# Optimization experiments

Hardware: AMD Instinct MI355X
Metric: run time of the kernel (lower is better)

## Reference

```python
import jax, jax.numpy as jnp
import numpy as np

ITERS = 3          # num_iterations
EPS_ATTN = 1e-8    # epsilon offset on attention
LN_EPS = 1e-5      # torch LayerNorm default eps


def _ln(x, g, b):
    m = x.mean(-1, keepdims=True)
    v = ((x - m) ** 2).mean(-1, keepdims=True)
    return (x - m) * jax.lax.rsqrt(v + LN_EPS) * g + b


def setup_inputs() -> dict:
    key = jax.random.key(0)
    ks = jax.random.split(key, 16)
    B, N, D, S, H = 64, 4096, 64, 8, 128

    def lin_w(k, fan_in, fan_out):
        lim = (1.0 / fan_in) ** 0.5
        return jax.random.uniform(k, (fan_in, fan_out), minval=-lim, maxval=lim, dtype=jnp.float32)

    def lin_b(k, fan_in, fan_out):
        lim = (1.0 / fan_in) ** 0.5
        return jax.random.uniform(k, (fan_out,), minval=-lim, maxval=lim, dtype=jnp.float32)

    return {
        "inputs": jax.random.normal(ks[0], (B, N, D), dtype=jnp.float32),
        "noise": jax.random.normal(ks[1], (B, S, D), dtype=jnp.float32),
        "slots_mu": jax.random.normal(ks[2], (1, 1, D), dtype=jnp.float32),
        "slots_log_sigma": jax.random.uniform(ks[3], (1, 1, D), minval=-0.3, maxval=0.3, dtype=jnp.float32),
        "wq": lin_w(ks[4], D, D), "bq": lin_b(ks[4], D, D),
        "wk": lin_w(ks[5], D, D), "bk": lin_b(ks[5], D, D),
        "wv": lin_w(ks[6], D, D), "bv": lin_b(ks[6], D, D),
        "w_ih": lin_w(ks[7], D, 3 * D), "b_ih": lin_b(ks[7], D, 3 * D),
        "w_hh": lin_w(ks[8], D, 3 * D), "b_hh": lin_b(ks[8], D, 3 * D),
        "w1": lin_w(ks[9], D, H), "b1": lin_b(ks[9], D, H),
        "w2": lin_w(ks[10], H, D), "b2": lin_b(ks[10], H, D),
        "g_in": jnp.ones((D,), jnp.float32), "beta_in": jnp.zeros((D,), jnp.float32),
        "g_sl": jnp.ones((D,), jnp.float32), "beta_sl": jnp.zeros((D,), jnp.float32),
        "g_ff": jnp.ones((D,), jnp.float32), "beta_ff": jnp.zeros((D,), jnp.float32),
    }


def reference(inputs, noise, slots_mu, slots_log_sigma, wq, bq, wk, bk, wv, bv,
              w_ih, b_ih, w_hh, b_hh, w1, b1, w2, b2,
              g_in, beta_in, g_sl, beta_sl, g_ff, beta_ff):
    b, n, d = inputs.shape
    scale = d ** -0.5

    slots = slots_mu + jnp.exp(slots_log_sigma) * noise          # [b, S, d]
    x = _ln(inputs, g_in, beta_in)
    k = x @ wk + bk                                              # [b, n, d]
    v = x @ wv + bv                                              # [b, n, d]

    for _ in range(ITERS):
        slots_prev = slots
        q = _ln(slots, g_sl, beta_sl) @ wq + bq                  # [b, S, d]
        dots = jnp.einsum('bid,bjd->bij', q, k) * scale          # [b, S, n]
        attn = jax.nn.softmax(dots, axis=1) + EPS_ATTN           # softmax over slots
        attn = attn / attn.sum(-1, keepdims=True)                # renorm over inputs
        updates = jnp.einsum('bjd,bij->bid', v, attn)            # [b, S, d]

        # GRUCell (torch gate order: reset, update, new)
        gx = updates @ w_ih + b_ih
        gh = slots_prev @ w_hh + b_hh
        xr, xz, xn = jnp.split(gx, 3, axis=-1)
        hr, hz, hn = jnp.split(gh, 3, axis=-1)
        r = jax.nn.sigmoid(xr + hr)
        z = jax.nn.sigmoid(xz + hz)
        nw = jnp.tanh(xn + r * hn)
        slots = (1.0 - z) * nw + z * slots_prev

        # residual MLP
        ff = _ln(slots, g_ff, beta_ff)
        slots = slots + (jax.nn.relu(ff @ w1 + b1) @ w2 + b2)
    return slots
```

## Files before the change

### kernel.cpp

```cpp
#include <hip/hip_runtime.h>
#include <math.h>

#define LN_EPS 1e-5f
#define EPS_ATTN 1e-8f
#define SCALE 0.125f
#define CHUNKS 32

__device__ __forceinline__ float wsum64(float v) {
#pragma unroll
  for (int m = 1; m <= 32; m <<= 1) v += __shfl_xor(v, m, 64);
  return v;
}

__device__ __forceinline__ float red16(float v) {
  v += __int_as_float(__builtin_amdgcn_update_dpp(0, __float_as_int(v), 0xB1, 0xF, 0xF, true));
  v += __int_as_float(__builtin_amdgcn_update_dpp(0, __float_as_int(v), 0x4E, 0xF, 0xF, true));
  v += __int_as_float(__builtin_amdgcn_update_dpp(0, __float_as_int(v), 0x124, 0xF, 0xF, true));
  v += __int_as_float(__builtin_amdgcn_update_dpp(0, __float_as_int(v), 0x128, 0xF, 0xF, true));
  return v;
}

__global__ __launch_bounds__(64) void k_init(
    const float* __restrict__ noise, const float* __restrict__ mu,
    const float* __restrict__ lsig,
    const float* __restrict__ wq, const float* __restrict__ bq,
    const float* __restrict__ wk, const float* __restrict__ bk,
    const float* __restrict__ g_sl, const float* __restrict__ beta_sl,
    float* __restrict__ S_buf, float* __restrict__ qk, float* __restrict__ qb,
    float* __restrict__ acc, float* __restrict__ asum,
    float* __restrict__ M, float* __restrict__ cvec,
    float* __restrict__ uvec, float* __restrict__ s0v)
{
  int bi = blockIdx.x;
  int lane = threadIdx.x;
  if (bi < 512) {
    float sl = mu[lane] + __expf(lsig[lane]) * noise[bi * 64 + lane];
    S_buf[bi * 64 + lane] = sl;
    acc[bi * 64 + lane] = 0.0f;
    if (lane == 0) asum[bi] = 0.0f;

    float s  = wsum64(sl);
    float s2 = wsum64(sl * sl);
    float mean = s * (1.0f / 64.0f);
    float var  = s2 * (1.0f / 64.0f) - mean * mean;
    float rstd = rsqrtf(var + LN_EPS);
    float ln = (sl - mean) * rstd * g_sl[lane] + beta_sl[lane];

    float q = bq[lane];
#pragma unroll
    for (int t = 0; t < 64; ++t) q += __shfl(ln, t, 64) * wq[t * 64 + lane];
    float qkl = 0.0f;
#pragma unroll
    for (int d = 0; d < 64; ++d) qkl += __shfl(q, d, 64) * wk[lane * 64 + d];
    qk[bi * 64 + lane] = qkl * SCALE;
    float qbl = wsum64(q * bk[lane]);
    if (lane == 0) qb[bi] = qbl * SCALE;
  } else if (bi < 576) {
    int t = bi - 512;
    float wqv = wq[t * 64 + lane];
    float m = 0.0f;
#pragma unroll
    for (int d = 0; d < 64; ++d) m += __shfl(wqv, d, 64) * wk[lane * 64 + d];
    M[t * 64 + lane] = m * SCALE;
    float uv = wsum64(wqv * bk[lane]);
    if (lane == 0) uvec[t] = uv * SCALE;
  } else {
    float bqv = bq[lane];
    float cc = 0.0f;
#pragma unroll
    for (int j = 0; j < 64; ++j) cc += __shfl(bqv, j, 64) * wk[lane * 64 + j];
    cvec[lane] = cc * SCALE;
    float ss = wsum64(bq[lane] * bk[lane]);
    if (lane == 0) s0v[0] = ss * SCALE;
  }
}

__global__ __launch_bounds__(256) void k_main(
    const float* __restrict__ inputs,
    const float* __restrict__ g_in, const float* __restrict__ beta_in,
    const float* __restrict__ qk, const float* __restrict__ qb,
    float* __restrict__ acc, float* __restrict__ asum)
{
  __shared__ float lds_qk[512];
  __shared__ float lds_qb[8];
  __shared__ float lds_acc[4][512];
  __shared__ float lds_as[4][8];
  const int b = blockIdx.y;
  const int chunk = blockIdx.x;
  const int tid = threadIdx.x;
  const int lane = tid & 63;
  const int wave = tid >> 6;
  const int p = lane & 15;

  if (tid < 128)
    ((float4*)lds_qk)[tid] = ((const float4*)(qk + b * 512))[tid];
  if (tid >= 128 && tid < 136)
    lds_qb[tid - 128] = qb[b * 8 + (tid - 128)];

  float4 g4  = ((const float4*)g_in)[p];
  float4 be4 = ((const float4*)beta_in)[p];

  float4 accl[8];
  float asl[8];
#pragma unroll
  for (int i = 0; i < 8; ++i) { accl[i] = make_float4(0.f, 0.f, 0.f, 0.f); asl[i] = 0.f; }

  __syncthreads();

  const float4* in4 = (const float4*)(inputs + (size_t)b * 4096 * 64);
  const float4* qk4 = (const float4*)lds_qk;
  const int rb0 = chunk * 128 + wave * 8;

  for (int it = 0; it < 4; ++it) {
    float4 xa = in4[(rb0 + it * 32) * 16 + lane];
    float4 xb = in4[(rb0 + it * 32 + 4) * 16 + lane];

    float sA  = red16(xa.x + xa.y + xa.z + xa.w);
    float s2A = red16(xa.x * xa.x + xa.y * xa.y + xa.z * xa.z + xa.w * xa.w);
    float meanA = sA * 0.015625f;
    float varA  = s2A * 0.015625f - meanA * meanA;
    float rstdA = rsqrtf(varA + LN_EPS);
    float4 xlnA;
    xlnA.x = (xa.x - meanA) * rstdA * g4.x + be4.x;
    xlnA.y = (xa.y - meanA) * rstdA * g4.y + be4.y;
    xlnA.z = (xa.z - meanA) * rstdA * g4.z + be4.z;
    xlnA.w = (xa.w - meanA) * rstdA * g4.w + be4.w;

    float sB  = red16(xb.x + xb.y + xb.z + xb.w);
    float s2B = red16(xb.x * xb.x + xb.y * xb.y + xb.z * xb.z + xb.w * xb.w);
    float meanB = sB * 0.015625f;
    float varB  = s2B * 0.015625f - meanB * meanB;
    float rstdB = rsqrtf(varB + LN_EPS);
    float4 xlnB;
    xlnB.x = (xb.x - meanB) * rstdB * g4.x + be4.x;
    xlnB.y = (xb.y - meanB) * rstdB * g4.y + be4.y;
    xlnB.z = (xb.z - meanB) * rstdB * g4.z + be4.z;
    xlnB.w = (xb.w - meanB) * rstdB * g4.w + be4.w;

    float pvA[8], pvB[8];
    float psA = 0.0f, psB = 0.0f;
#pragma unroll
    for (int i = 0; i < 8; ++i) {
      float4 qv = qk4[i * 16 + p];
      float qbi = lds_qb[i];
      float da = xlnA.x * qv.x + xlnA.y * qv.y + xlnA.z * qv.z + xlnA.w * qv.w;
      float db = xlnB.x * qv.x + xlnB.y * qv.y + xlnB.z * qv.z + xlnB.w * qv.w;
      da = red16(da) + qbi;
      db = red16(db) + qbi;
      float ea = __expf(da);
      float eb = __expf(db);
      pvA[i] = ea; psA += ea;
      pvB[i] = eb; psB += eb;
    }
    float invA = __builtin_amdgcn_rcpf(psA);
    float invB = __builtin_amdgcn_rcpf(psB);
#pragma unroll
    for (int i = 0; i < 8; ++i) {
      float ppa = pvA[i] * invA + EPS_ATTN;
      float ppb = pvB[i] * invB + EPS_ATTN;
      asl[i] += ppa + ppb;
      accl[i].x += ppa * xlnA.x; accl[i].x += ppb * xlnB.x;
      accl[i].y += ppa * xlnA.y; accl[i].y += ppb * xlnB.y;
      accl[i].z += ppa * xlnA.z; accl[i].z += ppb * xlnB.z;
      accl[i].w += ppa * xlnA.w; accl[i].w += ppb * xlnB.w;
    }
  }

#pragma unroll
  for (int i = 0; i < 8; ++i) {
#pragma unroll
    for (int m = 16; m <= 32; m <<= 1) {
      accl[i].x += __shfl_xor(accl[i].x, m, 64);
      accl[i].y += __shfl_xor(accl[i].y, m, 64);
      accl[i].z += __shfl_xor(accl[i].z, m, 64);
      accl[i].w += __shfl_xor(accl[i].w, m, 64);
      asl[i]    += __shfl_xor(asl[i], m, 64);
    }
  }

  if (lane < 16) {
    float4* dst = (float4*)lds_acc[wave];
#pragma unroll
    for (int i = 0; i < 8; ++i) dst[i * 16 + p] = accl[i];
  }
  if (lane == 0) {
#pragma unroll
    for (int i = 0; i < 8; ++i) lds_as[wave][i] = asl[i];
  }
  __syncthreads();

  for (int f = tid; f < 512; f += 256) {
    float ssum = lds_acc[0][f] + lds_acc[1][f] + lds_acc[2][f] + lds_acc[3][f];
    atomicAdd(&acc[b * 512 + f], ssum);
  }
  if (tid < 8) {
    float ssum = lds_as[0][tid] + lds_as[1][tid] + lds_as[2][tid] + lds_as[3][tid];
    atomicAdd(&asum[b * 8 + tid], ssum);
  }
}

__global__ __launch_bounds__(256) void k_update(
    const float* __restrict__ S_in, float* __restrict__ S_out,
    float* __restrict__ acc, float* __restrict__ asum,
    const float* __restrict__ wv, const float* __restrict__ bv,
    const float* __restrict__ w_ih, const float* __restrict__ b_ih,
    const float* __restrict__ w_hh, const float* __restrict__ b_hh,
    const float* __restrict__ w1, const float* __restrict__ b1,
    const float* __restrict__ w2, const float* __restrict__ b2,
    const float* __restrict__ g_ff, const float* __restrict__ beta_ff,
    const float* __restrict__ M, const float* __restrict__ cvec,
    const float* __restrict__ uvec, const float* __restrict__ s0v,
    const float* __restrict__ g_sl, const float* __restrict__ beta_sl,
    float* __restrict__ qk, float* __restrict__ qb, int do_next)
{
  __shared__ float red[6][4][64];
  const int bi   = blockIdx.x;
  const int tid  = threadIdx.x;
  const int lane = tid & 63;
  const int w    = tid >> 6;
  const int e0   = w * 16;

  float asv = asum[bi];
  float v   = acc[bi * 64 + lane] / asv;
  float sp  = S_in[bi * 64 + lane];

  float up = 0.0f;
#pragma unroll
  for (int e = 0; e < 16; ++e) {
    float vv = __shfl(v, e0 + e, 64);
    up += vv * wv[(e0 + e) * 64 + lane];
  }
  red[0][w][lane] = up;
  __syncthreads();
  float upd = bv[lane] + red[0][0][lane] + red[0][1][lane]
                       + red[0][2][lane] + red[0][3][lane];

  float gxr = 0, gxz = 0, gxn = 0, ghr = 0, ghz = 0, ghn = 0;
#pragma unroll
  for (int e = 0; e < 16; ++e) {
    int ee = e0 + e;
    float uu = __shfl(upd, ee, 64);
    float hh = __shfl(sp, ee, 64);
    const float* wi = w_ih + ee * 192;
    const float* wh = w_hh + ee * 192;
    gxr += uu * wi[lane]; gxz += uu * wi[64 + lane]; gxn += uu * wi[128 + lane];
    ghr += hh * wh[lane]; ghz += hh * wh[64 + lane]; ghn += hh * wh[128 + lane];
  }
  __syncthreads();
  red[0][w][lane] = gxr; red[1][w][lane] = gxz; red[2][w][lane] = gxn;
  red[3][w][lane] = ghr; red[4][w][lane] = ghz; red[5][w][lane] = ghn;
  __syncthreads();
  gxr = b_ih[lane]       + red[0][0][lane] + red[0][1][lane] + red[0][2][lane] + red[0][3][lane];
  gxz = b_ih[64 + lane]  + red[1][0][lane] + red[1][1][lane] + red[1][2][lane] + red[1][3][lane];
  gxn = b_ih[128 + lane] + red[2][0][lane] + red[2][1][lane] + red[2][2][lane] + red[2][3][lane];
  ghr = b_hh[lane]       + red[3][0][lane] + red[3][1][lane] + red[3][2][lane] + red[3][3][lane];
  ghz = b_hh[64 + lane]  + red[4][0][lane] + red[4][1][lane] + red[4][2][lane] + red[4][3][lane];
  ghn = b_hh[128 + lane] + red[5][0][lane] + red[5][1][lane] + red[5][2][lane] + red[5][3][lane];

  float r  = 1.0f / (1.0f + __expf(-(gxr + ghr)));
  float z  = 1.0f / (1.0f + __expf(-(gxz + ghz)));
  float nw = tanhf(gxn + r * ghn);
  float sn = (1.0f - z) * nw + z * sp;

  float s  = wsum64(sn);
  float s2 = wsum64(sn * sn);
  float mean = s * (1.0f / 64.0f);
  float var  = s2 * (1.0f / 64.0f) - mean * mean;
  float rstd = rsqrtf(var + LN_EPS);
  float ff = (sn - mean) * rstd * g_ff[lane] + beta_ff[lane];

  float h1 = 0.0f, h2 = 0.0f;
#pragma unroll
  for (int e = 0; e < 16; ++e) {
    int ee = e0 + e;
    float f = __shfl(ff, ee, 64);
    h1 += f * w1[ee * 128 + lane];
    h2 += f * w1[ee * 128 + 64 + lane];
  }
  __syncthreads();
  red[0][w][lane] = h1; red[1][w][lane] = h2;
  __syncthreads();
  h1 = fmaxf(b1[lane]      + red[0][0][lane] + red[0][1][lane] + red[0][2][lane] + red[0][3][lane], 0.0f);
  h2 = fmaxf(b1[64 + lane] + red[1][0][lane] + red[1][1][lane] + red[1][2][lane] + red[1][3][lane], 0.0f);

  float po = 0.0f;
#pragma unroll
  for (int t = 0; t < 16; ++t) {
    int tt = e0 + t;
    po += __shfl(h1, tt, 64) * w2[tt * 64 + lane];
    po += __shfl(h2, tt, 64) * w2[(64 + tt) * 64 + lane];
  }
  __syncthreads();
  red[0][w][lane] = po;
  __syncthreads();
  float o = sn + b2[lane] + red[0][0][lane] + red[0][1][lane]
                          + red[0][2][lane] + red[0][3][lane];
  if (w == 0) S_out[bi * 64 + lane] = o;

  if (do_next && w == 0) {
    acc[bi * 64 + lane] = 0.0f;
    if (lane == 0) asum[bi] = 0.0f;
  }

  if (do_next) {
    float so  = wsum64(o);
    float so2 = wsum64(o * o);
    float mo  = so * (1.0f / 64.0f);
    float vo  = so2 * (1.0f / 64.0f) - mo * mo;
    float ro  = rsqrtf(vo + LN_EPS);
    float ln  = (o - mo) * ro * g_sl[lane] + beta_sl[lane];

    float pq = 0.0f;
#pragma unroll
    for (int t = 0; t < 16; ++t) {
      int tt = e0 + t;
      pq += __shfl(ln, tt, 64) * M[tt * 64 + lane];
    }
    __syncthreads();
    red[1][w][lane] = pq;
    __syncthreads();
    if (w == 0) {
      qk[bi * 64 + lane] = cvec[lane] + red[1][0][lane] + red[1][1][lane]
                                      + red[1][2][lane] + red[1][3][lane];
      float pb = wsum64(ln * uvec[lane]);
      if (lane == 0) qb[bi] = s0v[0] + pb;
    }
  }
}

extern "C" void kernel_launch(void* const* d_in, const int* in_sizes, int n_in,
                              void* d_out, int out_size, void* d_ws, size_t ws_size,
                              hipStream_t stream) {
  const float* inputs  = (const float*)d_in[0];
  const float* noise   = (const float*)d_in[1];
  const float* mu      = (const float*)d_in[2];
  const float* lsig    = (const float*)d_in[3];
  const float* wq      = (const float*)d_in[4];
  const float* bq      = (const float*)d_in[5];
  const float* wk      = (const float*)d_in[6];
  const float* bk      = (const float*)d_in[7];
  const float* wv      = (const float*)d_in[8];
  const float* bv      = (const float*)d_in[9];
  const float* w_ih    = (const float*)d_in[10];
  const float* b_ih    = (const float*)d_in[11];
  const float* w_hh    = (const float*)d_in[12];
  const float* b_hh    = (const float*)d_in[13];
  const float* w1      = (const float*)d_in[14];
  const float* b1      = (const float*)d_in[15];
  const float* w2      = (const float*)d_in[16];
  const float* b2      = (const float*)d_in[17];
  const float* g_in    = (const float*)d_in[18];
  const float* beta_in = (const float*)d_in[19];
  const float* g_sl    = (const float*)d_in[20];
  const float* beta_sl = (const float*)d_in[21];
  const float* g_ff    = (const float*)d_in[22];
  const float* beta_ff = (const float*)d_in[23];

  float* S_buf = (float*)d_ws;
  float* qk    = S_buf + 32768;
  float* qb    = qk + 32768;
  float* acc   = qb + 512;
  float* asum  = acc + 32768;
  float* M     = asum + 512;
  float* cvec  = M + 4096;
  float* uvec  = cvec + 64;
  float* s0v   = uvec + 64;
  float* out   = (float*)d_out;

  k_init<<<577, 64, 0, stream>>>(noise, mu, lsig, wq, bq, wk, bk,
                                 g_sl, beta_sl, S_buf, qk, qb, acc, asum,
                                 M, cvec, uvec, s0v);

  for (int t = 0; t < 3; ++t) {
    k_main<<<dim3(CHUNKS, 64), 256, 0, stream>>>(inputs, g_in, beta_in,
                                                 qk, qb, acc, asum);
    float* dst = (t == 2) ? out : S_buf;
    k_update<<<512, 256, 0, stream>>>(S_buf, dst, acc, asum, wv, bv,
                                      w_ih, b_ih, w_hh, b_hh, w1, b1, w2, b2,
                                      g_ff, beta_ff, M, cvec, uvec, s0v,
                                      g_sl, beta_sl, qk, qb, (t == 2) ? 0 : 1);
  }
}
```

Measured before the change: 229.3 us.

## Fuse all stages into one cooperative persistent kernel with grid syncs

```diff
diff --git a/kernel.cpp b/kernel.cpp
--- a/kernel.cpp
+++ b/kernel.cpp
@@ -1,10 +1,24 @@
 #include <hip/hip_runtime.h>
+#include <hip/hip_cooperative_groups.h>
 #include <math.h>
+
+namespace cg = cooperative_groups;
 
 #define LN_EPS 1e-5f
 #define EPS_ATTN 1e-8f
 #define SCALE 0.125f
-#define CHUNKS 32
+#define CHUNKS 16
+
+struct KArgs {
+  const float *inputs, *noise, *mu, *lsig;
+  const float *wq, *bq, *wk, *bk, *wv, *bv;
+  const float *w_ih, *b_ih, *w_hh, *b_hh;
+  const float *w1, *b1, *w2, *b2;
+  const float *g_in, *beta_in, *g_sl, *beta_sl, *g_ff, *beta_ff;
+  float *S_buf, *qk, *qb, *acc, *asum;
+  float *M, *cvec, *uvec, *s0v;
+  float *out;
+};
 
 __device__ __forceinline__ float wsum64(float v) {
 #pragma unroll
@@ -20,85 +34,68 @@
   return v;
 }
 
-__global__ __launch_bounds__(64) void k_init(
-    const float* __restrict__ noise, const float* __restrict__ mu,
-    const float* __restrict__ lsig,
-    const float* __restrict__ wq, const float* __restrict__ bq,
-    const float* __restrict__ wk, const float* __restrict__ bk,
-    const float* __restrict__ g_sl, const float* __restrict__ beta_sl,
-    float* __restrict__ S_buf, float* __restrict__ qk, float* __restrict__ qb,
-    float* __restrict__ acc, float* __restrict__ asum,
-    float* __restrict__ M, float* __restrict__ cvec,
-    float* __restrict__ uvec, float* __restrict__ s0v)
-{
-  int bi = blockIdx.x;
-  int lane = threadIdx.x;
+__device__ __forceinline__ float ald(const float* p) {
+  return __hip_atomic_load(p, __ATOMIC_RELAXED, __HIP_MEMORY_SCOPE_AGENT);
+}
+__device__ __forceinline__ void ast(float* p, float v) {
+  __hip_atomic_store(p, v, __ATOMIC_RELAXED, __HIP_MEMORY_SCOPE_AGENT);
+}
+
+__device__ void init_work(int bi, int lane, const KArgs& a) {
   if (bi < 512) {
-    float sl = mu[lane] + __expf(lsig[lane]) * noise[bi * 64 + lane];
-    S_buf[bi * 64 + lane] = sl;
-    acc[bi * 64 + lane] = 0.0f;
-    if (lane == 0) asum[bi] = 0.0f;
+    float sl = a.mu[lane] + __expf(a.lsig[lane]) * a.noise[bi * 64 + lane];
+    ast(a.S_buf + bi * 64 + lane, sl);
+    ast(a.acc + bi * 64 + lane, 0.0f);
+    if (lane == 0) ast(a.asum + bi, 0.0f);
 
     float s  = wsum64(sl);
     float s2 = wsum64(sl * sl);
     float mean = s * (1.0f / 64.0f);
     float var  = s2 * (1.0f / 64.0f) - mean * mean;
     float rstd = rsqrtf(var + LN_EPS);
-    float ln = (sl - mean) * rstd * g_sl[lane] + beta_sl[lane];
-
-    float q = bq[lane];
-#pragma unroll
-    for (int t = 0; t < 64; ++t) q += __shfl(ln, t, 64) * wq[t * 64 + lane];
+    float ln = (sl - mean) * rstd * a.g_sl[lane] + a.beta_sl[lane];
+
+    float q = a.bq[lane];
+#pragma unroll
+    for (int t = 0; t < 64; ++t) q += __shfl(ln, t, 64) * a.wq[t * 64 + lane];
     float qkl = 0.0f;
 #pragma unroll
-    for (int d = 0; d < 64; ++d) qkl += __shfl(q, d, 64) * wk[lane * 64 + d];
-    qk[bi * 64 + lane] = qkl * SCALE;
-    float qbl = wsum64(q * bk[lane]);
-    if (lane == 0) qb[bi] = qbl * SCALE;
+    for (int d = 0; d < 64; ++d) qkl += __shfl(q, d, 64) * a.wk[lane * 64 + d];
+    ast(a.qk + bi * 64 + lane, qkl * SCALE);
+    float qbl = wsum64(q * a.bk[lane]);
+    if (lane == 0) ast(a.qb + bi, qbl * SCALE);
   } else if (bi < 576) {
     int t = bi - 512;
-    float wqv = wq[t * 64 + lane];
+    float wqv = a.wq[t * 64 + lane];
     float m = 0.0f;
 #pragma unroll
-    for (int d = 0; d < 64; ++d) m += __shfl(wqv, d, 64) * wk[lane * 64 + d];
-    M[t * 64 + lane] = m * SCALE;
-    float uv = wsum64(wqv * bk[lane]);
-    if (lane == 0) uvec[t] = uv * SCALE;
+    for (int d = 0; d < 64; ++d) m += __shfl(wqv, d, 64) * a.wk[lane * 64 + d];
+    a.M[t * 64 + lane] = m * SCALE;
+    float uv = wsum64(wqv * a.bk[lane]);
+    if (lane == 0) a.uvec[t] = uv * SCALE;
   } else {
-    float bqv = bq[lane];
+    float bqv = a.bq[lane];
     float cc = 0.0f;
 #pragma unroll
-    for (int j = 0; j < 64; ++j) cc += __shfl(bqv, j, 64) * wk[lane * 64 + j];
-    cvec[lane] = cc * SCALE;
-    float ss = wsum64(bq[lane] * bk[lane]);
-    if (lane == 0) s0v[0] = ss * SCALE;
-  }
-}
-
-__global__ __launch_bounds__(256) void k_main(
-    const float* __restrict__ inputs,
-    const float* __restrict__ g_in, const float* __restrict__ beta_in,
-    const float* __restrict__ qk, const float* __restrict__ qb,
-    float* __restrict__ acc, float* __restrict__ asum)
-{
-  __shared__ float lds_qk[512];
-  __shared__ float lds_qb[8];
-  __shared__ float lds_acc[4][512];
-  __shared__ float lds_as[4][8];
-  const int b = blockIdx.y;
-  const int chunk = blockIdx.x;
-  const int tid = threadIdx.x;
+    for (int j = 0; j < 64; ++j) cc += __shfl(bqv, j, 64) * a.wk[lane * 64 + j];
+    a.cvec[lane] = cc * SCALE;
+    float ss = wsum64(a.bq[lane] * a.bk[lane]);
+    if (lane == 0) a.s0v[0] = ss * SCALE;
+  }
+}
+
+__device__ void stream_work(int b, int chunk, int tid, const KArgs& a,
+                            float* lds_qk, float* lds_qb,
+                            float (*lds_acc)[512], float (*lds_as)[8]) {
   const int lane = tid & 63;
   const int wave = tid >> 6;
   const int p = lane & 15;
 
-  if (tid < 128)
-    ((float4*)lds_qk)[tid] = ((const float4*)(qk + b * 512))[tid];
-  if (tid >= 128 && tid < 136)
-    lds_qb[tid - 128] = qb[b * 8 + (tid - 128)];
-
-  float4 g4  = ((const float4*)g_in)[p];
-  float4 be4 = ((const float4*)beta_in)[p];
+  for (int i = tid; i < 512; i += 256) lds_qk[i] = ald(a.qk + b * 512 + i);
+  if (tid < 8) lds_qb[tid] = ald(a.qb + b * 8 + tid);
+
+  float4 g4  = ((const float4*)a.g_in)[p];
+  float4 be4 = ((const float4*)a.beta_in)[p];
 
   float4 accl[8];
   float asl[8];
@@ -107,11 +104,11 @@
 
   __syncthreads();
 
-  const float4* in4 = (const float4*)(inputs + (size_t)b * 4096 * 64);
+  const float4* in4 = (const float4*)(a.inputs + (size_t)b * 4096 * 64);
   const float4* qk4 = (const float4*)lds_qk;
-  const int rb0 = chunk * 128 + wave * 8;
-
-  for (int it = 0; it < 4; ++it) {
+  const int rb0 = chunk * 256 + wave * 8;
+
+  for (int it = 0; it < 8; ++it) {
     float4 xa = in4[(rb0 + it * 32) * 16 + lane];
     float4 xb = in4[(rb0 + it * 32 + 4) * 16 + lane];
 
@@ -191,49 +188,36 @@
 
   for (int f = tid; f < 512; f += 256) {
     float ssum = lds_acc[0][f] + lds_acc[1][f] + lds_acc[2][f] + lds_acc[3][f];
-    atomicAdd(&acc[b * 512 + f], ssum);
+    atomicAdd(&a.acc[b * 512 + f], ssum);
   }
   if (tid < 8) {
     float ssum = lds_as[0][tid] + lds_as[1][tid] + lds_as[2][tid] + lds_as[3][tid];
-    atomicAdd(&asum[b * 8 + tid], ssum);
-  }
-}
-
-__global__ __launch_bounds__(256) void k_update(
-    const float* __restrict__ S_in, float* __restrict__ S_out,
-    float* __restrict__ acc, float* __restrict__ asum,
-    const float* __restrict__ wv, const float* __restrict__ bv,
-    const float* __restrict__ w_ih, const float* __restrict__ b_ih,
-    const float* __restrict__ w_hh, const float* __restrict__ b_hh,
-    const float* __restrict__ w1, const float* __restrict__ b1,
-    const float* __restrict__ w2, const float* __restrict__ b2,
-    const float* __restrict__ g_ff, const float* __restrict__ beta_ff,
-    const float* __restrict__ M, const float* __restrict__ cvec,
-    const float* __restrict__ uvec, const float* __restrict__ s0v,
-    const float* __restrict__ g_sl, const float* __restrict__ beta_sl,
-    float* __restrict__ qk, float* __restrict__ qb, int do_next)
-{
-  __shared__ float red[6][4][64];
-  const int bi   = blockIdx.x;
-  const int tid  = threadIdx.x;
+    atomicAdd(&a.asum[b * 8 + tid], ssum);
+  }
+}
+
+__device__ void update_work(int bi, int do_next, float* dstS, int tid,
+                            const KArgs& a, float (*red)[4][64]) {
   const int lane = tid & 63;
   const int w    = tid >> 6;
   const int e0   = w * 16;
 
-  float asv = asum[bi];
-  float v   = acc[bi * 64 + lane] / asv;
-  float sp  = S_in[bi * 64 + lane];
+  __syncthreads();
+
+  float asv = ald(a.asum + bi);
+  float v   = ald(a.acc + bi * 64 + lane) / asv;
+  float sp  = ald(a.S_buf + bi * 64 + lane);
 
   float up = 0.0f;
 #pragma unroll
   for (int e = 0; e < 16; ++e) {
     float vv = __shfl(v, e0 + e, 64);
-    up += vv * wv[(e0 + e) * 64 + lane];
+    up += vv * a.wv[(e0 + e) * 64 + lane];
   }
   red[0][w][lane] = up;
   __syncthreads();
-  float upd = bv[lane] + red[0][0][lane] + red[0][1][lane]
-                       + red[0][2][lane] + red[0][3][lane];
+  float upd = a.bv[lane] + red[0][0][lane] + red[0][1][lane]
+                         + red[0][2][lane] + red[0][3][lane];
 
   float gxr = 0, gxz = 0, gxn = 0, ghr = 0, ghz = 0, ghn = 0;
 #pragma unroll
@@ -241,8 +225,8 @@
     int ee = e0 + e;
     float uu = __shfl(upd, ee, 64);
     float hh = __shfl(sp, ee, 64);
-    const float* wi = w_ih + ee * 192;
-    const float* wh = w_hh + ee * 192;
+    const float* wi = a.w_ih + ee * 192;
+    const float* wh = a.w_hh + ee * 192;
     gxr += uu * wi[lane]; gxz += uu * wi[64 + lane]; gxn += uu * wi[128 + lane];
     ghr += hh * wh[lane]; ghz += hh * wh[64 + lane]; ghn += hh * wh[128 + lane];
   }
@@ -250,12 +234,12 @@
   red[0][w][lane] = gxr; red[1][w][lane] = gxz; red[2][w][lane] = gxn;
   red[3][w][lane] = ghr; red[4][w][lane] = ghz; red[5][w][lane] = ghn;
   __syncthreads();
-  gxr = b_ih[lane]       + red[0][0][lane] + red[0][1][lane] + red[0][2][lane] + red[0][3][lane];
-  gxz = b_ih[64 + lane]  + red[1][0][lane] + red[1][1][lane] + red[1][2][lane] + red[1][3][lane];
-  gxn = b_ih[128 + lane] + red[2][0][lane] + red[2][1][lane] + red[2][2][lane] + red[2][3][lane];
-  ghr = b_hh[lane]       + red[3][0][lane] + red[3][1][lane] + red[3][2][lane] + red[3][3][lane];
-  ghz = b_hh[64 + lane]  + red[4][0][lane] + red[4][1][lane] + red[4][2][lane] + red[4][3][lane];
-  ghn = b_hh[128 + lane] + red[5][0][lane] + red[5][1][lane] + red[5][2][lane] + red[5][3][lane];
+  gxr = a.b_ih[lane]       + red[0][0][lane] + red[0][1][lane] + red[0][2][lane] + red[0][3][lane];
+  gxz = a.b_ih[64 + lane]  + red[1][0][lane] + red[1][1][lane] + red[1][2][lane] + red[1][3][lane];
+  gxn = a.b_ih[128 + lane] + red[2][0][lane] + red[2][1][lane] + red[2][2][lane] + red[2][3][lane];
+  ghr = a.b_hh[lane]       + red[3][0][lane] + red[3][1][lane] + red[3][2][lane] + red[3][3][lane];
+  ghz = a.b_hh[64 + lane]  + red[4][0][lane] + red[4][1][lane] + red[4][2][lane] + red[4][3][lane];
+  ghn = a.b_hh[128 + lane] + red[5][0][lane] + red[5][1][lane] + red[5][2][lane] + red[5][3][lane];
 
   float r  = 1.0f / (1.0f + __expf(-(gxr + ghr)));
   float z  = 1.0f / (1.0f + __expf(-(gxz + ghz)));
@@ -267,39 +251,39 @@
   float mean = s * (1.0f / 64.0f);
   float var  = s2 * (1.0f / 64.0f) - mean * mean;
   float rstd = rsqrtf(var + LN_EPS);
-  float ff = (sn - mean) * rstd * g_ff[lane] + beta_ff[lane];
+  float ff = (sn - mean) * rstd * a.g_ff[lane] + a.beta_ff[lane];
 
   float h1 = 0.0f, h2 = 0.0f;
 #pragma unroll
   for (int e = 0; e < 16; ++e) {
     int ee = e0 + e;
     float f = __shfl(ff, ee, 64);
-    h1 += f * w1[ee * 128 + lane];
-    h2 += f * w1[ee * 128 + 64 + lane];
+    h1 += f * a.w1[ee * 128 + lane];
+    h2 += f * a.w1[ee * 128 + 64 + lane];
   }
   __syncthreads();
   red[0][w][lane] = h1; red[1][w][lane] = h2;
   __syncthreads();
-  h1 = fmaxf(b1[lane]      + red[0][0][lane] + red[0][1][lane] + red[0][2][lane] + red[0][3][lane], 0.0f);
-  h2 = fmaxf(b1[64 + lane] + red[1][0][lane] + red[1][1][lane] + red[1][2][lane] + red[1][3][lane], 0.0f);
+  h1 = fmaxf(a.b1[lane]      + red[0][0][lane] + red[0][1][lane] + red[0][2][lane] + red[0][3][lane], 0.0f);
+  h2 = fmaxf(a.b1[64 + lane] + red[1][0][lane] + red[1][1][lane] + red[1][2][lane] + red[1][3][lane], 0.0f);
 
   float po = 0.0f;
 #pragma unroll
   for (int t = 0; t < 16; ++t) {
     int tt = e0 + t;
-    po += __shfl(h1, tt, 64) * w2[tt * 64 + lane];
-    po += __shfl(h2, tt, 64) * w2[(64 + tt) * 64 + lane];
+    po += __shfl(h1, tt, 64) * a.w2[tt * 64 + lane];
+    po += __shfl(h2, tt, 64) * a.w2[(64 + tt) * 64 + lane];
   }
   __syncthreads();
   red[0][w][lane] = po;
   __syncthreads();
-  float o = sn + b2[lane] + red[0][0][lane] + red[0][1][lane]
-                          + red[0][2][lane] + red[0][3][lane];
-  if (w == 0) S_out[bi * 64 + lane] = o;
+  float o = sn + a.b2[lane] + red[0][0][lane] + red[0][1][lane]
+                            + red[0][2][lane] + red[0][3][lane];
+  if (w == 0) ast(dstS + bi * 64 + lane, o);
 
   if (do_next && w == 0) {
-    acc[bi * 64 + lane] = 0.0f;
-    if (lane == 0) asum[bi] = 0.0f;
+    ast(a.acc + bi * 64 + lane, 0.0f);
+    if (lane == 0) ast(a.asum + bi, 0.0f);
   }
 
   if (do_next) {
@@ -308,76 +292,132 @@
     float mo  = so * (1.0f / 64.0f);
     float vo  = so2 * (1.0f / 64.0f) - mo * mo;
     float ro  = rsqrtf(vo + LN_EPS);
-    float ln  = (o - mo) * ro * g_sl[lane] + beta_sl[lane];
+    float ln  = (o - mo) * ro * a.g_sl[lane] + a.beta_sl[lane];
 
     float pq = 0.0f;
 #pragma unroll
     for (int t = 0; t < 16; ++t) {
       int tt = e0 + t;
-      pq += __shfl(ln, tt, 64) * M[tt * 64 + lane];
+      pq += __shfl(ln, tt, 64) * a.M[tt * 64 + lane];
     }
     __syncthreads();
     red[1][w][lane] = pq;
     __syncthreads();
     if (w == 0) {
-      qk[bi * 64 + lane] = cvec[lane] + red[1][0][lane] + red[1][1][lane]
-                                      + red[1][2][lane] + red[1][3][lane];
-      float pb = wsum64(ln * uvec[lane]);
-      if (lane == 0) qb[bi] = s0v[0] + pb;
-    }
-  }
+      ast(a.qk + bi * 64 + lane,
+          a.cvec[lane] + red[1][0][lane] + red[1][1][lane]
+                       + red[1][2][lane] + red[1][3][lane]);
+      float pb = wsum64(ln * a.uvec[lane]);
+      if (lane == 0) ast(a.qb + bi, a.s0v[0] + pb);
+    }
+  }
+}
+
+__global__ __launch_bounds__(256) void k_coop(KArgs a) {
+  __shared__ float lds_qk[512];
+  __shared__ float lds_qb[8];
+  __shared__ float lds_acc[4][512];
+  __shared__ float lds_as[4][8];
+  cg::grid_group grid = cg::this_grid();
+  const int tid = threadIdx.x;
+  const int nb = gridDim.x;
+
+  for (int w = blockIdx.x * 4 + (tid >> 6); w < 577; w += nb * 4)
+    init_work(w, tid & 63, a);
+  grid.sync();
+
+  for (int t = 0; t < 3; ++t) {
+    for (int w = blockIdx.x; w < 64 * CHUNKS; w += nb)
+      stream_work(w >> 4, w & (CHUNKS - 1), tid, a, lds_qk, lds_qb, lds_acc, lds_as);
+    grid.sync();
+    float* dst = (t == 2) ? a.out : a.S_buf;
+    for (int u = blockIdx.x; u < 512; u += nb)
+      update_work(u, (t < 2) ? 1 : 0, dst, tid, a, (float(*)[4][64])lds_acc);
+    if (t < 2) grid.sync();
+  }
+}
+
+__global__ __launch_bounds__(64) void k_init_sep(KArgs a) {
+  init_work(blockIdx.x, threadIdx.x, a);
+}
+__global__ __launch_bounds__(256) void k_main_sep(KArgs a) {
+  __shared__ float lds_qk[512];
+  __shared__ float lds_qb[8];
+  __shared__ float lds_acc[4][512];
+  __shared__ float lds_as[4][8];
+  stream_work(blockIdx.y, blockIdx.x, threadIdx.x, a, lds_qk, lds_qb, lds_acc, lds_as);
+}
+__global__ __launch_bounds__(256) void k_update_sep(KArgs a, int t) {
+  __shared__ float red[6][4][64];
+  update_work(blockIdx.x, (t < 2) ? 1 : 0, (t == 2) ? a.out : a.S_buf,
+              threadIdx.x, a, red);
 }
 
 extern "C" void kernel_launch(void* const* d_in, const int* in_sizes, int n_in,
                               void* d_out, int out_size, void* d_ws, size_t ws_size,
                               hipStream_t stream) {
-  const float* inputs  = (const float*)d_in[0];
-  const float* noise   = (const float*)d_in[1];
-  const float* mu      = (const float*)d_in[2];
-  const float* lsig    = (const float*)d_in[3];
-  const float* wq      = (const float*)d_in[4];
-  const float* bq      = (const float*)d_in[5];
-  const float* wk      = (const float*)d_in[6];
-  const float* bk      = (const float*)d_in[7];
-  const float* wv      = (const float*)d_in[8];
-  const float* bv      = (const float*)d_in[9];
-  const float* w_ih    = (const float*)d_in[10];
-  const float* b_ih    = (const float*)d_in[11];
-  const float* w_hh    = (const float*)d_in[12];
-  const float* b_hh    = (const float*)d_in[13];
-  const float* w1      = (const float*)d_in[14];
-  const float* b1      = (const float*)d_in[15];
-  const float* w2      = (const float*)d_in[16];
-  const float* b2      = (const float*)d_in[17];
-  const float* g_in    = (const float*)d_in[18];
-  const float* beta_in = (const float*)d_in[19];
-  const float* g_sl    = (const float*)d_in[20];
-  const float* beta_sl = (const float*)d_in[21];
-  const float* g_ff    = (const float*)d_in[22];
-  const float* beta_ff = (const float*)d_in[23];
-
-  float* S_buf = (float*)d_ws;
-  float* qk    = S_buf + 32768;
-  float* qb    = qk + 32768;
-  float* acc   = qb + 512;
-  float* asum  = acc + 32768;
-  float* M     = asum + 512;
-  float* cvec  = M + 4096;
-  float* uvec  = cvec + 64;
-  float* s0v   = uvec + 64;
-  float* out   = (float*)d_out;
-
-  k_init<<<577, 64, 0, stream>>>(noise, mu, lsig, wq, bq, wk, bk,
-                                 g_sl, beta_sl, S_buf, qk, qb, acc, asum,
-                                 M, cvec, uvec, s0v);
-
-  for (int t = 0; t < 3; ++t) {
-    k_main<<<dim3(CHUNKS, 64), 256, 0, stream>>>(inputs, g_in, beta_in,
-                                                 qk, qb, acc, asum);
-    float* dst = (t == 2) ? out : S_buf;
-    k_update<<<512, 256, 0, stream>>>(S_buf, dst, acc, asum, wv, bv,
-                                      w_ih, b_ih, w_hh, b_hh, w1, b1, w2, b2,
-                                      g_ff, beta_ff, M, cvec, uvec, s0v,
-                                      g_sl, beta_sl, qk, qb, (t == 2) ? 0 : 1);
-  }
-}
+  KArgs a;
+  a.inputs  = (const float*)d_in[0];
+  a.noise   = (const float*)d_in[1];
+  a.mu      = (const float*)d_in[2];
+  a.lsig    = (const float*)d_in[3];
+  a.wq      = (const float*)d_in[4];
+  a.bq      = (const float*)d_in[5];
+  a.wk      = (const float*)d_in[6];
+  a.bk      = (const float*)d_in[7];
+  a.wv      = (const float*)d_in[8];
+  a.bv      = (const float*)d_in[9];
+  a.w_ih    = (const float*)d_in[10];
+  a.b_ih    = (const float*)d_in[11];
+  a.w_hh    = (const float*)d_in[12];
+  a.b_hh    = (const float*)d_in[13];
+  a.w1      = (const float*)d_in[14];
+  a.b1      = (const float*)d_in[15];
+  a.w2      = (const float*)d_in[16];
+  a.b2      = (const float*)d_in[17];
+  a.g_in    = (const float*)d_in[18];
+  a.beta_in = (const float*)d_in[19];
+  a.g_sl    = (const float*)d_in[20];
+  a.beta_sl = (const float*)d_in[21];
+  a.g_ff    = (const float*)d_in[22];
+  a.beta_ff = (const float*)d_in[23];
+
+  float* ws = (float*)d_ws;
+  a.S_buf = ws;
+  a.qk    = ws + 32768;
+  a.qb    = a.qk + 32768;
+  a.acc   = a.qb + 512;
+  a.asum  = a.acc + 32768;
+  a.M     = a.asum + 512;
+  a.cvec  = a.M + 4096;
+  a.uvec  = a.cvec + 64;
+  a.s0v   = a.uvec + 64;
+  a.out   = (float*)d_out;
+
+  bool coop_ok = false;
+  int nb = 0;
+  if (hipOccupancyMaxActiveBlocksPerMultiprocessor(
+          &nb, (const void*)k_coop, 256, 0) == hipSuccess && nb >= 1) {
+    int ncu = 256;
+    hipDeviceProp_t prop;
+    int dev = 0;
+    if (hipGetDevice(&dev) == hipSuccess &&
+        hipGetDeviceProperties(&prop, dev) == hipSuccess &&
+        prop.multiProcessorCount > 0)
+      ncu = prop.multiProcessorCount;
+    int grid = nb * ncu;
+    if (grid > 64 * CHUNKS) grid = 64 * CHUNKS;
+    void* args[] = { (void*)&a };
+    if (hipLaunchCooperativeKernel((const void*)k_coop, dim3(grid), dim3(256),
+                                   args, 0, stream) == hipSuccess)
+      coop_ok = true;
+  }
+
+  if (!coop_ok) {
+    k_init_sep<<<577, 64, 0, stream>>>(a);
+    for (int t = 0; t < 3; ++t) {
+      k_main_sep<<<dim3(CHUNKS, 64), 256, 0, stream>>>(a);
+      k_update_sep<<<512, 256, 0, stream>>>(a, t);
+    }
+  }
+}
```

New measurement: 229.4 us. No clear change (+0.0%).
